# Kernel tuning notes

Hardware: AMD Instinct MI355X
Metric: run time of the kernel (lower is better)

## Reference

```python
import jax, jax.numpy as jnp
import numpy as np
from jax import lax

T, B, C, HW = 64, 32, 4, 84
HID, A, FEAT = 256, 12, 1152  # 6*6*32 after 4 stride-2 convs on 84x84


def _conv(x, w, b):
    # NCHW input, OIHW kernel, stride 2, padding 1 (matches nn.Conv2d(k=3,s=2,p=1))
    y = lax.conv_general_dilated(x, w, (2, 2), ((1, 1), (1, 1)),
                                 dimension_numbers=('NCHW', 'OIHW', 'NCHW'))
    return y + b[None, :, None, None]


def setup_inputs() -> dict:
    key = jax.random.key(0)
    ks = jax.random.split(key, 16)
    inputs = jax.random.normal(ks[0], (T, B, C, HW, HW), dtype=jnp.float32)
    rnn_in = jax.random.normal(ks[1], (B, HID), dtype=jnp.float32)
    mask = jnp.ones((T, B, 1), dtype=jnp.float32)
    actions = jax.random.randint(ks[2], (T * B,), 0, A)
    s = 0.05
    w1 = jax.random.normal(ks[3], (32, C, 3, 3), jnp.float32) * s
    w2 = jax.random.normal(ks[4], (32, 32, 3, 3), jnp.float32) * s
    w3 = jax.random.normal(ks[5], (32, 32, 3, 3), jnp.float32) * s
    w4 = jax.random.normal(ks[6], (32, 32, 3, 3), jnp.float32) * s
    b1 = jnp.zeros((32,), jnp.float32); b2 = jnp.zeros((32,), jnp.float32)
    b3 = jnp.zeros((32,), jnp.float32); b4 = jnp.zeros((32,), jnp.float32)
    W_ih = jax.random.normal(ks[7], (3 * HID, FEAT), jnp.float32) * 0.02
    W_hh = jax.random.normal(ks[8], (3 * HID, HID), jnp.float32) * 0.02
    b_ih = jnp.zeros((3 * HID,), jnp.float32)
    b_hh = jnp.zeros((3 * HID,), jnp.float32)
    Wc = jax.random.normal(ks[9], (1, HID), jnp.float32) * 0.06
    bc = jnp.zeros((1,), jnp.float32)
    Wa = jax.random.normal(ks[10], (A, HID), jnp.float32) * 0.01
    ba = jnp.zeros((A,), jnp.float32)
    return {"inputs": inputs, "rnn_in": rnn_in, "mask": mask, "actions": actions,
            "w1": w1, "b1": b1, "w2": w2, "b2": b2, "w3": w3, "b3": b3,
            "w4": w4, "b4": b4, "W_ih": W_ih, "W_hh": W_hh, "b_ih": b_ih,
            "b_hh": b_hh, "Wc": Wc, "bc": bc, "Wa": Wa, "ba": ba}


def reference(inputs, rnn_in, mask, actions, w1, b1, w2, b2, w3, b3, w4, b4,
              W_ih, W_hh, b_ih, b_hh, Wc, bc, Wa, ba):
    Tl, Bl = inputs.shape[0], inputs.shape[1]
    x = inputs.reshape(Tl * Bl, inputs.shape[2], inputs.shape[3], inputs.shape[4])
    for w, b in ((w1, b1), (w2, b2), (w3, b3), (w4, b4)):
        x = jax.nn.elu(_conv(x, w, b))
    x = x.reshape(Tl, Bl, -1)  # [T, B, FEAT]

    def step(h, xm):
        x_t, m_t = xm
        h = h * m_t  # masked hidden reset
        gi = x_t @ W_ih.T + b_ih
        gh = h @ W_hh.T + b_hh
        i_r, i_z, i_n = jnp.split(gi, 3, axis=-1)
        h_r, h_z, h_n = jnp.split(gh, 3, axis=-1)
        r = jax.nn.sigmoid(i_r + h_r)
        z = jax.nn.sigmoid(i_z + h_z)
        n = jnp.tanh(i_n + r * h_n)
        h_new = (1.0 - z) * n + z * h
        return h_new, h_new

    h_final, outs = lax.scan(step, rnn_in, (x, mask))
    out = outs.reshape(Tl * Bl, HID)

    v = (out @ Wc.T + bc)[:, 0]
    logits = out @ Wa.T + ba
    logp = jax.nn.log_softmax(logits, axis=-1)
    logp_a = jnp.take_along_axis(logp, actions[:, None], axis=1)[:, 0]
    ent = -jnp.sum(jnp.exp(logp) * logp, axis=-1)
    return (v, actions, logp_a, ent, h_final)
```

## Files before the change

### kernel.cpp

```cpp
#include <hip/hip_runtime.h>
#include <hip/hip_bf16.h>
#include <math.h>

#define TT 64
#define BB 32
#define HID 256
#define NA 12
#define FEAT 1152
#define NB 2048
#define G3 768

typedef __hip_bfloat16 bf16;
typedef __attribute__((ext_vector_type(8))) short short8;
typedef __attribute__((ext_vector_type(4))) float f32x4;

static __device__ __forceinline__ float bf2f(bf16 v) { return __bfloat162float(v); }
static __device__ __forceinline__ bf16 f2bf(float v) { return __float2bfloat16(v); }

#define MFMA(a, b, c) __builtin_amdgcn_mfma_f32_16x16x32_bf16((a), (b), (c), 0, 0, 0)

__global__ __launch_bounds__(256) void prep_kernel(
    const float* __restrict__ w1, const float* __restrict__ w2,
    const float* __restrict__ w3, const float* __restrict__ w4,
    const float* __restrict__ W_ih, const float* __restrict__ W_hh,
    const float* __restrict__ b_ih, const float* __restrict__ b_hh,
    bf16* __restrict__ wB1, bf16* __restrict__ wB2,
    bf16* __restrict__ wB3, bf16* __restrict__ wB4,
    bf16* __restrict__ wihF, bf16* __restrict__ whhB, float* __restrict__ biasg)
{
    int i = blockIdx.x * 256 + threadIdx.x;
    if (i < 2048) {
        int j = i & 7, l = (i >> 3) & 63, rest = i >> 9;
        int ch = rest & 1, nt = rest >> 1;
        int k = ch * 32 + 8 * (l >> 4) + j;
        int co = nt * 16 + (l & 15);
        wB1[i] = f2bf(k < 36 ? w1[co * 36 + (k & 3) * 9 + (k >> 2)] : 0.0f);
    }
    if (i < 9216) {
        int j = i & 7, l = (i >> 3) & 63, rest = i >> 9;
        int kk = rest % 9, nt = rest / 9;
        int ci = 8 * (l >> 4) + j, co = nt * 16 + (l & 15);
        wB2[i] = f2bf(w2[co * 288 + ci * 9 + kk]);
        wB3[i] = f2bf(w3[co * 288 + ci * 9 + kk]);
        wB4[i] = f2bf(w4[co * 288 + ci * 9 + kk]);
    }
    if (i < 884736) {
        int j = i & 7, l = (i >> 3) & 63, rest = i >> 9;
        int st = rest % 48, ch = rest / 48;
        int k = ch * 32 + 8 * (l >> 4) + j, n = st * 16 + (l & 15);
        wihF[i] = f2bf(W_ih[(size_t)n * FEAT + k]);
    }
    if (i < 196608) {
        int k = i / G3, g = i % G3;
        whhB[i] = f2bf(W_hh[(size_t)g * HID + k]);
    }
    if (i < G3) biasg[i] = b_ih[i] + (i < 2 * HID ? b_hh[i] : 0.0f);
}

__global__ __launch_bounds__(256) void conv1_kernel(
    const float* __restrict__ in, int n0,
    const bf16* __restrict__ wB1g, const float* __restrict__ b1,
    bf16* __restrict__ x1)
{
    __shared__ bf16 ins[7 * 84 * 4];
    __shared__ bf16 A[64 * 72];
    __shared__ bf16 wBs[2048];
    int tid = threadIdx.x;
    int nl = blockIdx.x / 28, blk = blockIdx.x % 28;
    int n = n0 + nl;
    int p0 = blk * 64;
    int oy_lo = p0 / 42;
    int oy_hi = (p0 + 63) / 42; if (oy_hi > 41) oy_hi = 41;
    int y_lo = 2 * oy_lo - 1;
    int rows = 2 * oy_hi + 2 - y_lo;

    if (tid < 256) ((uint4*)wBs)[tid] = ((const uint4*)wB1g)[tid];
    const float* inb = in + (size_t)n * 4 * 7056;
    for (int i = tid; i < rows * 336; i += 256) {
        int r = i / 336, rem = i % 336, ci = rem / 84, x = rem % 84;
        int y = y_lo + r;
        float v = (y >= 0) ? inb[ci * 7056 + y * 84 + x] : 0.0f;
        ins[(r * 84 + x) * 4 + ci] = f2bf(v);
    }
    __syncthreads();
    for (int i = tid; i < 576; i += 256) {
        int m = i / 9, q = i % 9;
        uint2 z; z.x = 0u; z.y = 0u;
        *(uint2*)&A[m * 72 + 36 + q * 4] = z;
    }
    for (int i = tid; i < 576; i += 256) {
        int m = i / 9, kk = i % 9;
        int kh = kk / 3, kw = kk - kh * 3;
        int p = p0 + m;
        uint2 v; v.x = 0u; v.y = 0u;
        if (p < 1764) {
            int oy = p / 42, ox = p - oy * 42;
            int y = 2 * oy - 1 + kh, x = 2 * ox - 1 + kw;
            if ((unsigned)y < 84u && (unsigned)x < 84u)
                v = *(const uint2*)&ins[((y - y_lo) * 84 + x) * 4];
        }
        *(uint2*)&A[m * 72 + kk * 4] = v;
    }
    __syncthreads();
    int lane = tid & 63, g = tid >> 6, quad = lane >> 4, c16 = lane & 15;
    int ma = g * 16 + c16;
    short8 a0 = *(const short8*)&A[ma * 72 + quad * 8];
    short8 a1 = *(const short8*)&A[ma * 72 + 32 + quad * 8];
    #pragma unroll
    for (int nt = 0; nt < 2; nt++) {
        float bv = b1[nt * 16 + c16];
        f32x4 acc = {bv, bv, bv, bv};
        short8 b0 = *(const short8*)&wBs[((nt * 2 + 0) * 64 + lane) * 8];
        short8 bq = *(const short8*)&wBs[((nt * 2 + 1) * 64 + lane) * 8];
        acc = MFMA(a0, b0, acc);
        acc = MFMA(a1, bq, acc);
        #pragma unroll
        for (int r = 0; r < 4; r++) {
            int p = p0 + g * 16 + 4 * quad + r;
            if (p < 1764) {
                float v = acc[r];
                v = v > 0.0f ? v : expm1f(v);
                x1[((size_t)nl * 1764 + p) * 32 + nt * 16 + c16] = f2bf(v);
            }
        }
    }
}

template<int HI, int HO, int OUTMODE>
__global__ __launch_bounds__(256) void convN_kernel(
    const bf16* __restrict__ xin, bf16* __restrict__ xout,
    const bf16* __restrict__ wBg, const float* __restrict__ bias, int n0)
{
    constexpr int NPIX = HO * HO;
    constexpr int NBLK = (NPIX + 63) / 64;
    __shared__ bf16 A[64 * 296];
    __shared__ bf16 wBs[9216];
    int tid = threadIdx.x;
    int nl = blockIdx.x / NBLK, blk = blockIdx.x % NBLK;
    int p0 = blk * 64;
    for (int i = tid; i < 1152; i += 256) ((uint4*)wBs)[i] = ((const uint4*)wBg)[i];
    const bf16* xb = xin + (size_t)nl * HI * HI * 32;
    for (int i = tid; i < 2304; i += 256) {
        int m = i / 36, t = i % 36, kk = t >> 2, part = t & 3;
        int kh = kk / 3, kw = kk - kh * 3;
        int p = p0 + m;
        uint4 v; v.x = v.y = v.z = v.w = 0u;
        if (p < NPIX) {
            int oy = p / HO, ox = p - oy * HO;
            int y = 2 * oy - 1 + kh, x = 2 * ox - 1 + kw;
            if ((unsigned)y < (unsigned)HI && (unsigned)x < (unsigned)HI)
                v = *(const uint4*)&xb[((size_t)(y * HI + x)) * 32 + part * 8];
        }
        *(uint4*)&A[m * 296 + kk * 32 + part * 8] = v;
    }
    __syncthreads();
    int lane = tid & 63, g = tid >> 6, quad = lane >> 4, c16 = lane & 15;
    int ma = g * 16 + c16;
    short8 af[9];
    #pragma unroll
    for (int kk = 0; kk < 9; kk++)
        af[kk] = *(const short8*)&A[ma * 296 + kk * 32 + quad * 8];
    #pragma unroll
    for (int nt = 0; nt < 2; nt++) {
        float bv = bias[nt * 16 + c16];
        f32x4 acc = {bv, bv, bv, bv};
        #pragma unroll
        for (int kk = 0; kk < 9; kk++) {
            short8 bfr = *(const short8*)&wBs[((nt * 9 + kk) * 64 + lane) * 8];
            acc = MFMA(af[kk], bfr, acc);
        }
        #pragma unroll
        for (int r = 0; r < 4; r++) {
            int p = p0 + g * 16 + 4 * quad + r;
            if (p < NPIX) {
                float v = acc[r];
                v = v > 0.0f ? v : expm1f(v);
                if (OUTMODE == 0)
                    xout[(((size_t)(n0 + nl)) * NPIX + p) * 32 + nt * 16 + c16] = f2bf(v);
                else
                    xout[(size_t)(n0 + nl) * FEAT + (nt * 16 + c16) * 36 + p] = f2bf(v);
            }
        }
    }
}

__global__ __launch_bounds__(256) void gemm_gi_kernel(
    const bf16* __restrict__ X, const bf16* __restrict__ wihF,
    const float* __restrict__ biasg, float* __restrict__ GI)
{
    __shared__ bf16 As[64 * 40];
    int tid = threadIdx.x;
    int m0 = blockIdx.x * 64, nb = blockIdx.y * 4, n0 = blockIdx.y * 64;
    int lane = tid & 63, g = tid >> 6, quad = lane >> 4, c16 = lane & 15;
    f32x4 acc[4];
    #pragma unroll
    for (int st = 0; st < 4; st++) {
        float bv = biasg[n0 + st * 16 + c16];
        acc[st] = (f32x4){bv, bv, bv, bv};
    }
    int sm = tid >> 2, sp = tid & 3;
    for (int ch = 0; ch < 36; ch++) {
        __syncthreads();
        *(uint4*)&As[sm * 40 + sp * 8] =
            *(const uint4*)&X[(size_t)(m0 + sm) * FEAT + ch * 32 + sp * 8];
        __syncthreads();
        short8 af = *(const short8*)&As[(g * 16 + c16) * 40 + quad * 8];
        #pragma unroll
        for (int st = 0; st < 4; st++) {
            short8 bfr = *(const short8*)&wihF[(((size_t)ch * 48 + nb + st) * 64 + lane) * 8];
            acc[st] = MFMA(af, bfr, acc[st]);
        }
    }
    #pragma unroll
    for (int st = 0; st < 4; st++)
        #pragma unroll
        for (int r = 0; r < 4; r++)
            GI[(size_t)(m0 + g * 16 + 4 * quad + r) * G3 + n0 + st * 16 + c16] = acc[st][r];
}

__global__ __launch_bounds__(256) void scan_kernel(
    const float* __restrict__ GI, const bf16* __restrict__ whhB,
    const float* __restrict__ b_hh, const float* __restrict__ rnn_in,
    const float* __restrict__ mask, float* __restrict__ H)
{
    __shared__ float hs[HID];
    int b = blockIdx.x, j = threadIdx.x;
    float h = rnn_in[b * HID + j];
    float bhn = b_hh[2 * HID + j];
    for (int t = 0; t < TT; t++) {
        float m = mask[t * BB + b];
        h *= m;
        hs[j] = h;
        __syncthreads();
        float ar = 0.f, az = 0.f, an = 0.f;
        #pragma unroll 4
        for (int k = 0; k < HID; k++) {
            float hk = hs[k];
            const bf16* wp = whhB + (size_t)k * G3 + j;
            ar += hk * bf2f(wp[0]);
            az += hk * bf2f(wp[256]);
            an += hk * bf2f(wp[512]);
        }
        int row = t * BB + b;
        const float* gp = GI + (size_t)row * G3 + j;
        float r = 1.0f / (1.0f + expf(-(gp[0] + ar)));
        float z = 1.0f / (1.0f + expf(-(gp[256] + az)));
        float pre = gp[512] + r * (an + bhn);
        pre = fminf(15.0f, fmaxf(-15.0f, pre));
        float e = expf(2.0f * pre);
        float nn = (e - 1.0f) / (e + 1.0f);
        h = (1.0f - z) * nn + z * h;
        H[(size_t)row * HID + j] = h;
        __syncthreads();
    }
}

__global__ __launch_bounds__(256) void heads_kernel(
    const float* __restrict__ H, const int* __restrict__ actions,
    const float* __restrict__ Wc, const float* __restrict__ bc,
    const float* __restrict__ Wa, const float* __restrict__ ba,
    float* __restrict__ out)
{
    int r = blockIdx.x * 256 + threadIdx.x;
    if (r >= NB) return;
    const float* h = H + (size_t)r * HID;
    float v = bc[0];
    for (int k = 0; k < HID; k++) v += h[k] * Wc[k];
    float lg[NA];
    for (int a = 0; a < NA; a++) {
        float s = ba[a];
        const float* wa = Wa + a * HID;
        for (int k = 0; k < HID; k++) s += h[k] * wa[k];
        lg[a] = s;
    }
    float mx = lg[0];
    for (int a = 1; a < NA; a++) mx = fmaxf(mx, lg[a]);
    float Z = 0.f;
    for (int a = 0; a < NA; a++) Z += expf(lg[a] - mx);
    float lse = mx + logf(Z);
    int act = actions[r];
    float logp_a = lg[act] - lse;
    float ent = 0.f;
    for (int a = 0; a < NA; a++) {
        float lp = lg[a] - lse;
        ent -= expf(lp) * lp;
    }
    out[r]          = v;
    out[NB + r]     = (float)act;
    out[2 * NB + r] = logp_a;
    out[3 * NB + r] = ent;
}

__global__ __launch_bounds__(256) void hfin_kernel(const float* __restrict__ H, float* __restrict__ out)
{
    int i = blockIdx.x * 256 + threadIdx.x;
    if (i < BB * HID)
        out[4 * NB + i] = H[(size_t)(TT - 1) * BB * HID + i];
}

extern "C" void kernel_launch(void* const* d_in, const int* in_sizes, int n_in,
                              void* d_out, int out_size, void* d_ws, size_t ws_size,
                              hipStream_t stream) {
    const float* inputs  = (const float*)d_in[0];
    const float* rnn_in  = (const float*)d_in[1];
    const float* mask    = (const float*)d_in[2];
    const int*   actions = (const int*)d_in[3];
    const float* w1 = (const float*)d_in[4];
    const float* b1 = (const float*)d_in[5];
    const float* w2 = (const float*)d_in[6];
    const float* b2 = (const float*)d_in[7];
    const float* w3 = (const float*)d_in[8];
    const float* b3 = (const float*)d_in[9];
    const float* w4 = (const float*)d_in[10];
    const float* b4 = (const float*)d_in[11];
    const float* W_ih = (const float*)d_in[12];
    const float* W_hh = (const float*)d_in[13];
    const float* b_ih = (const float*)d_in[14];
    const float* b_hh = (const float*)d_in[15];
    const float* Wc = (const float*)d_in[16];
    const float* bc = (const float*)d_in[17];
    const float* Wa = (const float*)d_in[18];
    const float* ba = (const float*)d_in[19];
    float* out = (float*)d_out;

    char* ws = (char*)d_ws;
    size_t o = 0;
    auto nxt = [&](size_t b) { void* p = ws + o; o += (b + 255) & ~(size_t)255; return p; };
    bf16* wB1  = (bf16*)nxt(2048 * 2);
    bf16* wB2  = (bf16*)nxt(9216 * 2);
    bf16* wB3  = (bf16*)nxt(9216 * 2);
    bf16* wB4  = (bf16*)nxt(9216 * 2);
    bf16* wihF = (bf16*)nxt(884736 * 2);
    bf16* whhB = (bf16*)nxt(196608 * 2);
    float* biasg = (float*)nxt(768 * 4);
    bf16* x4 = (bf16*)nxt((size_t)NB * FEAT * 2);
    bf16* x2 = (bf16*)nxt((size_t)NB * 441 * 32 * 2);
    char* R1 = (char*)nxt(28901376);
    bf16*  x1c = (bf16*)R1;
    bf16*  x3  = (bf16*)R1;
    float* GI  = (float*)(R1 + 15859712);
    float* H   = (float*)(R1 + 15859712 + 6291456);

    prep_kernel<<<3456, 256, 0, stream>>>(w1, w2, w3, w4, W_ih, W_hh, b_ih, b_hh,
                                          wB1, wB2, wB3, wB4, wihF, whhB, biasg);
    for (int c = 0; c < 8; c++) {
        conv1_kernel<<<256 * 28, 256, 0, stream>>>(inputs, c * 256, wB1, b1, x1c);
        convN_kernel<42, 21, 0><<<256 * 7, 256, 0, stream>>>(x1c, x2, wB2, b2, c * 256);
    }
    convN_kernel<21, 11, 0><<<2048 * 2, 256, 0, stream>>>(x2, x3, wB3, b3, 0);
    convN_kernel<11, 6, 1><<<2048, 256, 0, stream>>>(x3, x4, wB4, b4, 0);
    gemm_gi_kernel<<<dim3(32, 12), 256, 0, stream>>>(x4, wihF, biasg, GI);
    scan_kernel<<<BB, HID, 0, stream>>>(GI, whhB, b_hh, rnn_in, mask, H);
    heads_kernel<<<NB / 256, 256, 0, stream>>>(H, actions, Wc, bc, Wa, ba, out);
    hfin_kernel<<<(BB * HID + 255) / 256, 256, 0, stream>>>(H, out);
}
```

Baseline: 1.822 ms.

## Keep GRU recurrent weights in registers with 768 threads; enlarge conv1 chunks

The scan kernel now runs 768 threads per batch element, one per gate output. Each thread holds its bf16 row of W_hh in registers and computes the dot product from shared memory, so the weights are no longer re-read from global memory on every time step. The next step's mask is folded into the hidden-state write, and the gates are combined through shared memory. Separately, the conv1/conv2 chunk size is chosen from the available workspace (up to all 2048 images), which cuts the number of kernel launches. The cost is heavy register pressure from the 128 registers of weights per thread, plus a larger workspace footprint.

```diff
diff --git a/kernel.cpp b/kernel.cpp
--- a/kernel.cpp
+++ b/kernel.cpp
@@ -26,7 +26,7 @@
     const float* __restrict__ b_ih, const float* __restrict__ b_hh,
     bf16* __restrict__ wB1, bf16* __restrict__ wB2,
     bf16* __restrict__ wB3, bf16* __restrict__ wB4,
-    bf16* __restrict__ wihF, bf16* __restrict__ whhB, float* __restrict__ biasg)
+    bf16* __restrict__ wihF, bf16* __restrict__ whh16, float* __restrict__ biasg)
 {
     int i = blockIdx.x * 256 + threadIdx.x;
     if (i < 2048) {
@@ -51,8 +51,7 @@
         wihF[i] = f2bf(W_ih[(size_t)n * FEAT + k]);
     }
     if (i < 196608) {
-        int k = i / G3, g = i % G3;
-        whhB[i] = f2bf(W_hh[(size_t)g * HID + k]);
+        whh16[i] = f2bf(W_hh[i]);
     }
     if (i < G3) biasg[i] = b_ih[i] + (i < 2 * HID ? b_hh[i] : 0.0f);
 }
@@ -218,39 +217,66 @@
             GI[(size_t)(m0 + g * 16 + 4 * quad + r) * G3 + n0 + st * 16 + c16] = acc[st][r];
 }
 
-__global__ __launch_bounds__(256) void scan_kernel(
-    const float* __restrict__ GI, const bf16* __restrict__ whhB,
+__global__ __launch_bounds__(768, 3) void scan_kernel(
+    const float* __restrict__ GI, const bf16* __restrict__ whh16,
     const float* __restrict__ b_hh, const float* __restrict__ rnn_in,
     const float* __restrict__ mask, float* __restrict__ H)
 {
     __shared__ float hs[HID];
-    int b = blockIdx.x, j = threadIdx.x;
-    float h = rnn_in[b * HID + j];
-    float bhn = b_hh[2 * HID + j];
-    for (int t = 0; t < TT; t++) {
-        float m = mask[t * BB + b];
-        h *= m;
-        hs[j] = h;
+    __shared__ float pr[HID];
+    __shared__ float pz[HID];
+    __shared__ float pn[HID];
+    int b = blockIdx.x, t = threadIdx.x;
+    int gate = t >> 8, j = t & 255;
+
+    uint4 wreg[32];
+    const uint4* wrow = (const uint4*)(whh16 + (size_t)t * HID);
+    #pragma unroll
+    for (int kc = 0; kc < 32; kc++) wreg[kc] = wrow[kc];
+
+    float bhn = (gate == 2) ? b_hh[2 * HID + j] : 0.0f;
+    if (t < HID) hs[t] = rnn_in[b * HID + t] * mask[b];
+    __syncthreads();
+
+    for (int step = 0; step < TT; step++) {
+        int row = step * BB + b;
+        float gr = 0.f, gz = 0.f, gn = 0.f, hold = 0.f, mnext = 1.0f;
+        if (gate == 0) {
+            const float* gp = GI + (size_t)row * G3 + j;
+            gr = gp[0]; gz = gp[256]; gn = gp[512];
+            hold = hs[j];
+            if (step + 1 < TT) mnext = mask[(step + 1) * BB + b];
+        }
+        float acc = bhn;
+        #pragma unroll
+        for (int kc = 0; kc < 32; kc++) {
+            uint4 w = wreg[kc];
+            float4 h0 = *(const float4*)&hs[kc * 8];
+            float4 h1 = *(const float4*)&hs[kc * 8 + 4];
+            acc = fmaf(h0.x, __uint_as_float(w.x << 16), acc);
+            acc = fmaf(h0.y, __uint_as_float(w.x & 0xffff0000u), acc);
+            acc = fmaf(h0.z, __uint_as_float(w.y << 16), acc);
+            acc = fmaf(h0.w, __uint_as_float(w.y & 0xffff0000u), acc);
+            acc = fmaf(h1.x, __uint_as_float(w.z << 16), acc);
+            acc = fmaf(h1.y, __uint_as_float(w.z & 0xffff0000u), acc);
+            acc = fmaf(h1.z, __uint_as_float(w.w << 16), acc);
+            acc = fmaf(h1.w, __uint_as_float(w.w & 0xffff0000u), acc);
+        }
+        if (gate == 0)      pr[j] = acc;
+        else if (gate == 1) pz[j] = acc;
+        else                pn[j] = acc;
         __syncthreads();
-        float ar = 0.f, az = 0.f, an = 0.f;
-        #pragma unroll 4
-        for (int k = 0; k < HID; k++) {
-            float hk = hs[k];
-            const bf16* wp = whhB + (size_t)k * G3 + j;
-            ar += hk * bf2f(wp[0]);
-            az += hk * bf2f(wp[256]);
-            an += hk * bf2f(wp[512]);
-        }
-        int row = t * BB + b;
-        const float* gp = GI + (size_t)row * G3 + j;
-        float r = 1.0f / (1.0f + expf(-(gp[0] + ar)));
-        float z = 1.0f / (1.0f + expf(-(gp[256] + az)));
-        float pre = gp[512] + r * (an + bhn);
-        pre = fminf(15.0f, fmaxf(-15.0f, pre));
-        float e = expf(2.0f * pre);
-        float nn = (e - 1.0f) / (e + 1.0f);
-        h = (1.0f - z) * nn + z * h;
-        H[(size_t)row * HID + j] = h;
+        if (gate == 0) {
+            float r = 1.0f / (1.0f + expf(-(gr + pr[j])));
+            float z = 1.0f / (1.0f + expf(-(gz + pz[j])));
+            float pre = gn + r * pn[j];
+            pre = fminf(15.0f, fmaxf(-15.0f, pre));
+            float e = expf(2.0f * pre);
+            float nn = (e - 1.0f) / (e + 1.0f);
+            float hnew = (1.0f - z) * nn + z * hold;
+            H[(size_t)row * HID + j] = hnew;
+            hs[j] = hnew * mnext;
+        }
         __syncthreads();
     }
 }
@@ -331,26 +357,46 @@
     bf16* wB3  = (bf16*)nxt(9216 * 2);
     bf16* wB4  = (bf16*)nxt(9216 * 2);
     bf16* wihF = (bf16*)nxt(884736 * 2);
-    bf16* whhB = (bf16*)nxt(196608 * 2);
+    bf16* whh16 = (bf16*)nxt(196608 * 2);
     float* biasg = (float*)nxt(768 * 4);
     bf16* x4 = (bf16*)nxt((size_t)NB * FEAT * 2);
     bf16* x2 = (bf16*)nxt((size_t)NB * 441 * 32 * 2);
-    char* R1 = (char*)nxt(28901376);
-    bf16*  x1c = (bf16*)R1;
-    bf16*  x3  = (bf16*)R1;
-    float* GI  = (float*)(R1 + 15859712);
-    float* H   = (float*)(R1 + 15859712 + 6291456);
+
+    const size_t X1_PER_IMG = 1764 * 32 * 2;
+    const size_t TAILFIX = 15859712 + 6291456 + 2097152 + 1024;
+    bf16* x3; float* GI; float* H; bf16* x1c;
+    int CH;
+    if (ws_size >= o + TAILFIX + 2048 * X1_PER_IMG + (1u << 20)) {
+        CH = 2048;
+        x3 = (bf16*)nxt(15859712); GI = (float*)nxt(6291456); H = (float*)nxt(2097152);
+        x1c = (bf16*)nxt(2048 * X1_PER_IMG);
+    } else if (ws_size >= o + TAILFIX + 512 * X1_PER_IMG + (1u << 20)) {
+        CH = 512;
+        x3 = (bf16*)nxt(15859712); GI = (float*)nxt(6291456); H = (float*)nxt(2097152);
+        x1c = (bf16*)nxt(512 * X1_PER_IMG);
+    } else if (ws_size >= o + TAILFIX + 256 * X1_PER_IMG + (1u << 20)) {
+        CH = 256;
+        x3 = (bf16*)nxt(15859712); GI = (float*)nxt(6291456); H = (float*)nxt(2097152);
+        x1c = (bf16*)nxt(256 * X1_PER_IMG);
+    } else {
+        CH = 256;
+        char* R1 = (char*)nxt(28901376);
+        x1c = (bf16*)R1;
+        x3  = (bf16*)R1;
+        GI  = (float*)(R1 + 15859712);
+        H   = (float*)(R1 + 15859712 + 6291456);
+    }
 
     prep_kernel<<<3456, 256, 0, stream>>>(w1, w2, w3, w4, W_ih, W_hh, b_ih, b_hh,
-                                          wB1, wB2, wB3, wB4, wihF, whhB, biasg);
-    for (int c = 0; c < 8; c++) {
-        conv1_kernel<<<256 * 28, 256, 0, stream>>>(inputs, c * 256, wB1, b1, x1c);
-        convN_kernel<42, 21, 0><<<256 * 7, 256, 0, stream>>>(x1c, x2, wB2, b2, c * 256);
+                                          wB1, wB2, wB3, wB4, wihF, whh16, biasg);
+    for (int c = 0; c < 2048 / CH; c++) {
+        conv1_kernel<<<CH * 28, 256, 0, stream>>>(inputs, c * CH, wB1, b1, x1c);
+        convN_kernel<42, 21, 0><<<CH * 7, 256, 0, stream>>>(x1c, x2, wB2, b2, c * CH);
     }
     convN_kernel<21, 11, 0><<<2048 * 2, 256, 0, stream>>>(x2, x3, wB3, b3, 0);
     convN_kernel<11, 6, 1><<<2048, 256, 0, stream>>>(x3, x4, wB4, b4, 0);
     gemm_gi_kernel<<<dim3(32, 12), 256, 0, stream>>>(x4, wihF, biasg, GI);
-    scan_kernel<<<BB, HID, 0, stream>>>(GI, whhB, b_hh, rnn_in, mask, H);
+    scan_kernel<<<BB, 768, 0, stream>>>(GI, whh16, b_hh, rnn_in, mask, H);
     heads_kernel<<<NB / 256, 256, 0, stream>>>(H, actions, Wc, bc, Wa, ba, out);
     hfin_kernel<<<(BB * HID + 255) / 256, 256, 0, stream>>>(H, out);
 }
```

After: 1.705 ms. 1.07x faster.
